# Optimization experiments

Measured on AMD Instinct MI355X. Metric: run time of the kernel, lower is better.

## Reference

```python
import jax, jax.numpy as jnp
import numpy as np

BS = 131072
NX = 4       # num_dim_x (p, theta, v, omega)
NU = 1       # num_dim_control
H = 256      # n_hidden


def segway_dynamics(x):
    # x: [bs, 4] -> f: [bs, 4], g: [bs, 4, 1]
    theta, v, omega = x[:, 1], x[:, 2], x[:, 3]
    c, s = jnp.cos(theta), jnp.sin(theta)
    f2 = (c * (9.8 * s + 11.5 * v) + 68.4 * v - 1.2 * omega ** 2 * s) / (c - 24.7)
    f3 = (-58.8 * v * c - 243.5 * v - s * (208.3 + omega ** 2 * c)) / (c ** 2 - 24.7)
    f = jnp.stack([v, omega, f2, f3], axis=1)
    g2 = (-1.8 * c - 10.9) / (c - 24.7)
    g3 = (9.3 * c + 38.6) / (c ** 2 - 24.7)
    zero = jnp.zeros_like(g2)
    g = jnp.stack([zero, zero, g2, g3], axis=1)[:, :, None]
    return f, g


def setup_inputs() -> dict:
    key = jax.random.key(0)
    ks = jax.random.split(key, 13)
    d = {"x": jax.random.normal(ks[0], (BS, NX), dtype=jnp.float32)}
    shapes = {
        "Vw1": (H, NX), "Vb1": (H,),
        "Vw2": (H, H),  "Vb2": (H,),
        "Vw3": (H // 4, H), "Vb3": (H // 4,),
        "Uw1": (H, NX), "Ub1": (H,),
        "Uw2": (H, H),  "Ub2": (H,),
        "Uw3": (NU, H), "Ub3": (NU,),
    }
    for i, (name, shp) in enumerate(shapes.items()):
        d[name] = jax.random.normal(ks[i + 1], shp, dtype=jnp.float32) * 0.05
    return d


def reference(x, Vw1, Vb1, Vw2, Vb2, Vw3, Vb3, Uw1, Ub1, Uw2, Ub2, Uw3, Ub3):
    # --- Lyapunov value + analytic gradient ---
    a1 = jnp.tanh(x @ Vw1.T + Vb1)          # [bs, H]
    a2 = jnp.tanh(a1 @ Vw2.T + Vb2)         # [bs, H]
    a3 = jnp.tanh(a2 @ Vw3.T + Vb3)         # [bs, H//4]
    V = 0.5 * jnp.sum(a3 * a3, axis=1)      # [bs]
    # diag_embed(1-tanh^2) @ W  ==  (1-tanh^2)[:, :, None] * W  (no dense diag)
    D1 = (1.0 - a1 ** 2)[:, :, None] * Vw1[None]                          # [bs, H, 4]
    D2 = (1.0 - a2 ** 2)[:, :, None] * jnp.einsum('ij,bjk->bik', Vw2, D1)  # [bs, H, 4]
    D3 = (1.0 - a3 ** 2)[:, :, None] * jnp.einsum('ij,bjk->bik', Vw3, D2)  # [bs, H/4, 4]
    grad_V = jnp.einsum('bi,bij->bj', a3, D3)  # [bs, 4]

    # --- learned controls ---
    u1 = jnp.tanh(x @ Uw1.T + Ub1)
    u2 = jnp.tanh(u1 @ Uw2.T + Ub2)
    u = jnp.tanh(u2 @ Uw3.T + Ub3) * 20.0     # [bs, 1]

    # --- Lie derivatives / Vdot ---
    f, g = segway_dynamics(x)
    L_f_V = jnp.sum(grad_V * f, axis=1, keepdims=True)    # [bs, 1]
    L_g_V = jnp.einsum('bi,bic->bc', grad_V, g)           # [bs, 1]
    Vdot = (L_f_V + jnp.sum(L_g_V * u, axis=1, keepdims=True))[:, :, None]  # [bs,1,1]
    return u, V, Vdot
```

## Files before the change

kernel.cpp:

```cpp
#include <hip/hip_runtime.h>
#include <hip/hip_bf16.h>

#define BSZ 131072

typedef __bf16 v8bf __attribute__((ext_vector_type(8)));
typedef float f32x4 __attribute__((ext_vector_type(4)));

constexpr int RPB = 32;
constexpr int MT  = RPB / 16;
constexpr int NTHREADS = 512;
constexpr int LDA = 264;

constexpr int OFF_B2T = 0;
constexpr int OFF_U2T = 65536;
constexpr int OFF_B2  = 131072;
constexpr int OFF_B3T = 196608;
constexpr int OFF_B3  = 212992;
constexpr int OFF_U3  = 229376;
constexpr int OFF_GV  = 233472;
constexpr int OFF_LV1 = 237568;
constexpr int OFF_LU1 = 245760;
constexpr int WS_ELEMS = 253952;

__device__ __forceinline__ float tanhf_fast(float x){
  float e = __builtin_amdgcn_exp2f(x * 2.885390082f);
  return __builtin_fmaf(-2.0f, __builtin_amdgcn_rcpf(e + 1.0f), 1.0f);
}

__device__ __forceinline__ __bf16 f2bf(float f){
  unsigned u = __builtin_bit_cast(unsigned, f);
  u += 0x8000u;
  unsigned short h = (unsigned short)(u >> 16);
  return __builtin_bit_cast(__bf16, h);
}

__device__ __forceinline__ unsigned pk2bf(float lo, float hi){
  unsigned r;
  asm("v_cvt_pk_bf16_f32 %0, %1, %2" : "=v"(r) : "v"(lo), "v"(hi));
  return r;
}
__device__ __forceinline__ float bflo(unsigned u){ return __builtin_bit_cast(float, u << 16); }
__device__ __forceinline__ float bfhi(unsigned u){ return __builtin_bit_cast(float, u & 0xffff0000u); }

__global__ void prep_weights(const float* __restrict__ Vw2,
                             const float* __restrict__ Uw2,
                             const float* __restrict__ Vw3,
                             const float* __restrict__ Vw1,
                             const float* __restrict__ Uw1,
                             const float* __restrict__ Uw3,
                             __bf16* __restrict__ ws){
  int e = blockIdx.x * 256 + threadIdx.x;
  if (e >= WS_ELEMS) return;
  int idx, NT, base, mode; const float* W;
  if      (e <  65536){ idx = e;          W = Vw2; mode = 0; NT = 16; base = OFF_B2T; }
  else if (e < 131072){ idx = e - 65536;  W = Uw2; mode = 0; NT = 16; base = OFF_U2T; }
  else if (e < 196608){ idx = e - 131072; W = Vw2; mode = 1; NT = 16; base = OFF_B2;  }
  else if (e < 212992){ idx = e - 196608; W = Vw3; mode = 0; NT = 4;  base = OFF_B3T; }
  else if (e < 229376){ idx = e - 212992; W = Vw3; mode = 1; NT = 16; base = OFF_B3;  }
  else if (e < 233472){ idx = e - 229376; W = Uw3; mode = 2; NT = 1;  base = OFF_U3;  }
  else if (e < 237568){ idx = e - 233472; W = Vw1; mode = 3; NT = 1;  base = OFF_GV;  }
  else if (e < 245760){ idx = e - 237568; W = Vw1; mode = 4; NT = 16; base = OFF_LV1; }
  else                { idx = e - 245760; W = Uw1; mode = 4; NT = 16; base = OFF_LU1; }
  int j = idx & 7, l = (idx >> 3) & 63, f = idx >> 9;
  int nt = f % NT, ks = f / NT;
  int k = ks * 32 + (l >> 4) * 8 + j;
  int n = nt * 16 + (l & 15);
  float v;
  if      (mode == 0) v = W[n * 256 + k];
  else if (mode == 1) v = W[k * 256 + n];
  else if (mode == 2) v = (n == 0) ? W[k] : 0.0f;
  else if (mode == 3) v = (n < 4)  ? W[k * 4 + n] : 0.0f;
  else                v = (k < 4)  ? W[n * 4 + k] : 0.0f;
  ws[base + idx] = f2bf(v);
}

__global__ __launch_bounds__(NTHREADS, 8) void fused_clf(
    const float* __restrict__ x,
    const float* __restrict__ Vb1, const float* __restrict__ Vb2,
    const float* __restrict__ Vb3,
    const float* __restrict__ Ub1, const float* __restrict__ Ub2,
    const float* __restrict__ Ub3, const float* __restrict__ Uw3,
    const __bf16* __restrict__ ws,
    float* __restrict__ out)
{
  __shared__ alignas(16) __bf16 b1[RPB][LDA];
  __shared__ alignas(16) __bf16 b2[RPB][LDA];
  __shared__ union alignas(16) S3 {
    __bf16 b3[RPB][72];
    float  r4[8][RPB][4];
  } s3;
  __shared__ alignas(16) float red[RPB][4];
  __shared__ float utile[RPB];

  const int tid  = threadIdx.x;
  const int lane = tid & 63;
  const int wave = tid >> 6;
  const int quad = lane >> 4;
  const int l16  = lane & 15;
  const int row0 = blockIdx.x * RPB;

  v8bf xa[MT];
  #pragma unroll
  for (int m = 0; m < MT; m++){
    v8bf z;
    #pragma unroll
    for (int j = 0; j < 8; j++) z[j] = (__bf16)0.0f;
    if (quad == 0){
      float4 xv = ((const float4*)x)[row0 + m*16 + l16];
      z[0] = f2bf(xv.x); z[1] = f2bf(xv.y); z[2] = f2bf(xv.z); z[3] = f2bf(xv.w);
    }
    xa[m] = z;
  }


  auto layer1m = [&](const __bf16* __restrict__ Bw, const float* __restrict__ bv,
                     __bf16 (*dst)[LDA]){
    const v8bf* B = (const v8bf*)Bw;
    v8bf bf0 = B[(wave*2 + 0)*64 + lane];
    v8bf bf1 = B[(wave*2 + 1)*64 + lane];
    f32x4 acc[MT][2];
    #pragma unroll
    for (int m = 0; m < MT; m++){ f32x4 z={0.f,0.f,0.f,0.f}; acc[m][0]=z; acc[m][1]=z; }
    __builtin_amdgcn_s_setprio(1);
    #pragma unroll
    for (int m = 0; m < MT; m++){
      acc[m][0] = __builtin_amdgcn_mfma_f32_16x16x32_bf16(bf0, xa[m], acc[m][0], 0,0,0);
      acc[m][1] = __builtin_amdgcn_mfma_f32_16x16x32_bf16(bf1, xa[m], acc[m][1], 0,0,0);
    }
    __builtin_amdgcn_s_setprio(0);
    #pragma unroll
    for (int nt = 0; nt < 2; nt++){
      const int f0 = (wave*2 + nt)*16 + quad*4;
      f32x4 bvv = ((const f32x4*)bv)[f0 >> 2];
      #pragma unroll
      for (int m = 0; m < MT; m++){
        const int brow = m*16 + l16;
        uint2 pk;
        pk.x = pk2bf(tanhf_fast(acc[m][nt][0] + bvv[0]),
                     tanhf_fast(acc[m][nt][1] + bvv[1]));
        pk.y = pk2bf(tanhf_fast(acc[m][nt][2] + bvv[2]),
                     tanhf_fast(acc[m][nt][3] + bvv[3]));
        *(uint2*)&dst[brow][f0] = pk;
      }
    }
  };

  auto gemm256 = [&](const __bf16 (*A)[LDA], const __bf16* __restrict__ Bw,
                     const float* __restrict__ bias, __bf16 (*dst)[LDA], int epi){
    f32x4 acc[MT][2];
    #pragma unroll
    for (int m = 0; m < MT; m++){ f32x4 z={0.f,0.f,0.f,0.f}; acc[m][0]=z; acc[m][1]=z; }
    const v8bf* B = (const v8bf*)Bw;
    __builtin_amdgcn_s_setprio(1);
    #pragma unroll
    for (int kk = 0; kk < 8; kk++){
      v8bf a[MT];
      #pragma unroll
      for (int m = 0; m < MT; m++)
        a[m] = *(const v8bf*)&A[m*16 + l16][kk*32 + quad*8];
      #pragma unroll
      for (int nt = 0; nt < 2; nt++){
        v8bf bf = B[(kk*16 + wave*2 + nt)*64 + lane];
        #pragma unroll
        for (int m = 0; m < MT; m++)
          acc[m][nt] = __builtin_amdgcn_mfma_f32_16x16x32_bf16(bf, a[m], acc[m][nt], 0,0,0);
      }
    }
    __builtin_amdgcn_s_setprio(0);
    #pragma unroll
    for (int nt = 0; nt < 2; nt++){
      const int f0 = (wave*2 + nt)*16 + quad*4;
      f32x4 bvv = {0.f,0.f,0.f,0.f};
      if (epi == 0) bvv = ((const f32x4*)bias)[f0 >> 2];
      #pragma unroll
      for (int m = 0; m < MT; m++){
        const int brow = m*16 + l16;
        uint2 pk;
        if (epi == 0){
          pk.x = pk2bf(tanhf_fast(acc[m][nt][0] + bvv[0]),
                       tanhf_fast(acc[m][nt][1] + bvv[1]));
          pk.y = pk2bf(tanhf_fast(acc[m][nt][2] + bvv[2]),
                       tanhf_fast(acc[m][nt][3] + bvv[3]));
        } else {
          uint2 old = *(const uint2*)&dst[brow][f0];
          float a0 = bflo(old.x), a1 = bfhi(old.x);
          float c0 = bflo(old.y), c1 = bfhi(old.y);
          pk.x = pk2bf(acc[m][nt][0] * (1.0f - a0*a0),
                       acc[m][nt][1] * (1.0f - a1*a1));
          pk.y = pk2bf(acc[m][nt][2] * (1.0f - c0*c0),
                       acc[m][nt][3] * (1.0f - c1*c1));
        }
        *(uint2*)&dst[brow][f0] = pk;
      }
    }
  };

  auto u2dot = [&](const __bf16 (*A)[LDA], const __bf16* __restrict__ Bw,
                   const float* __restrict__ bias, const float* __restrict__ w3){
    f32x4 acc[MT][2];
    #pragma unroll
    for (int m = 0; m < MT; m++){ f32x4 z={0.f,0.f,0.f,0.f}; acc[m][0]=z; acc[m][1]=z; }
    const v8bf* B = (const v8bf*)Bw;
    __builtin_amdgcn_s_setprio(1);
    #pragma unroll
    for (int kk = 0; kk < 8; kk++){
      v8bf a[MT];
      #pragma unroll
      for (int m = 0; m < MT; m++)
        a[m] = *(const v8bf*)&A[m*16 + l16][kk*32 + quad*8];
      #pragma unroll
      for (int nt = 0; nt < 2; nt++){
        v8bf bf = B[(kk*16 + wave*2 + nt)*64 + lane];
        #pragma unroll
        for (int m = 0; m < MT; m++)
          acc[m][nt] = __builtin_amdgcn_mfma_f32_16x16x32_bf16(bf, a[m], acc[m][nt], 0,0,0);
      }
    }
    __builtin_amdgcn_s_setprio(0);
    float part[MT];
    #pragma unroll
    for (int m = 0; m < MT; m++) part[m] = 0.f;
    #pragma unroll
    for (int nt = 0; nt < 2; nt++){
      const int f0 = (wave*2 + nt)*16 + quad*4;
      f32x4 bvv = ((const f32x4*)bias)[f0 >> 2];
      f32x4 w3v = ((const f32x4*)w3)[f0 >> 2];
      #pragma unroll
      for (int m = 0; m < MT; m++)
        #pragma unroll
        for (int r = 0; r < 4; r++)
          part[m] = __builtin_fmaf(tanhf_fast(acc[m][nt][r] + bvv[r]), w3v[r], part[m]);
    }
    #pragma unroll
    for (int m = 0; m < MT; m++){
      part[m] += __shfl_xor(part[m], 16);
      part[m] += __shfl_xor(part[m], 32);
    }
    if (quad == 0){
      #pragma unroll
      for (int m = 0; m < MT; m++)
        s3.r4[wave][m*16 + l16][0] = part[m];
    }
  };

  auto mfma_reduce4 = [&](const __bf16 (*A)[LDA], const __bf16* __restrict__ Bw){
    f32x4 acc[MT];
    #pragma unroll
    for (int m = 0; m < MT; m++){ f32x4 z={0.f,0.f,0.f,0.f}; acc[m]=z; }
    const v8bf* B = (const v8bf*)Bw;
    v8bf bf = B[wave*64 + lane];
    __builtin_amdgcn_s_setprio(1);
    #pragma unroll
    for (int m = 0; m < MT; m++){
      v8bf a = *(const v8bf*)&A[m*16 + l16][wave*32 + quad*8];
      acc[m] = __builtin_amdgcn_mfma_f32_16x16x32_bf16(bf, a, acc[m], 0,0,0);
    }
    __builtin_amdgcn_s_setprio(0);
    if (quad == 0){
      #pragma unroll
      for (int m = 0; m < MT; m++)
        *(f32x4*)&s3.r4[wave][m*16 + l16][0] = acc[m];
    }
  };

  layer1m(ws + OFF_LU1, Ub1, b2);
  layer1m(ws + OFF_LV1, Vb1, b1);
  __syncthreads();
  u2dot(b2, ws + OFF_U2T, Ub2, Uw3);
  __syncthreads();
  gemm256(b1, ws + OFF_B2T, Vb2, b2, 0);
  if (tid < RPB){
    float z = Ub3[0];
    #pragma unroll
    for (int w = 0; w < 8; w++) z += s3.r4[w][tid][0];
    float u = tanhf_fast(z) * 20.0f;
    utile[tid] = u;
    out[row0 + tid] = u;
  }
  __syncthreads();

  {
    const int mt = wave >> 2;
    const int nt = wave & 3;
    f32x4 acc = {0.f,0.f,0.f,0.f};
    const v8bf* B = (const v8bf*)(ws + OFF_B3T);
    __builtin_amdgcn_s_setprio(1);
    #pragma unroll
    for (int kk = 0; kk < 8; kk++){
      v8bf bf = B[(kk*4 + nt)*64 + lane];
      v8bf a = *(const v8bf*)&b2[mt*16 + l16][kk*32 + quad*8];
      acc = __builtin_amdgcn_mfma_f32_16x16x32_bf16(bf, a, acc, 0,0,0);
    }
    __builtin_amdgcn_s_setprio(0);
    const int f0 = nt*16 + quad*4;
    f32x4 bvv = ((const f32x4*)Vb3)[f0 >> 2];
    const int brow = mt*16 + l16;
    float t0 = tanhf_fast(acc[0] + bvv[0]);
    float t1 = tanhf_fast(acc[1] + bvv[1]);
    float t2 = tanhf_fast(acc[2] + bvv[2]);
    float t3 = tanhf_fast(acc[3] + bvv[3]);
    float s0 = t0*t0, s1 = t1*t1, s2 = t2*t2, s3q = t3*t3;
    float sq = (s0 + s1) + (s2 + s3q);
    sq += __shfl_xor(sq, 16);
    sq += __shfl_xor(sq, 32);
    if (quad == 0) red[brow][nt] = sq;
    uint2 pk;
    pk.x = pk2bf(t0*(1.0f - s0), t1*(1.0f - s1));
    pk.y = pk2bf(t2*(1.0f - s2), t3*(1.0f - s3q));
    *(uint2*)&s3.b3[brow][f0] = pk;
  }
  __syncthreads();

  {
    f32x4 acc[MT][2];
    #pragma unroll
    for (int m = 0; m < MT; m++){ f32x4 z={0.f,0.f,0.f,0.f}; acc[m][0]=z; acc[m][1]=z; }
    const v8bf* B = (const v8bf*)(ws + OFF_B3);
    __builtin_amdgcn_s_setprio(1);
    #pragma unroll
    for (int kk = 0; kk < 2; kk++){
      v8bf a[MT];
      #pragma unroll
      for (int m = 0; m < MT; m++)
        a[m] = *(const v8bf*)&s3.b3[m*16 + l16][kk*32 + quad*8];
      #pragma unroll
      for (int nt = 0; nt < 2; nt++){
        v8bf bf = B[(kk*16 + wave*2 + nt)*64 + lane];
        #pragma unroll
        for (int m = 0; m < MT; m++)
          acc[m][nt] = __builtin_amdgcn_mfma_f32_16x16x32_bf16(bf, a[m], acc[m][nt], 0,0,0);
      }
    }
    __builtin_amdgcn_s_setprio(0);
    #pragma unroll
    for (int nt = 0; nt < 2; nt++){
      const int f0 = (wave*2 + nt)*16 + quad*4;
      #pragma unroll
      for (int m = 0; m < MT; m++){
        const int brow = m*16 + l16;
        uint2 old = *(const uint2*)&b2[brow][f0];
        float a0 = bflo(old.x), a1 = bfhi(old.x);
        float c0 = bflo(old.y), c1 = bfhi(old.y);
        uint2 pk;
        pk.x = pk2bf(acc[m][nt][0] * (1.0f - a0*a0),
                     acc[m][nt][1] * (1.0f - a1*a1));
        pk.y = pk2bf(acc[m][nt][2] * (1.0f - c0*c0),
                     acc[m][nt][3] * (1.0f - c1*c1));
        *(uint2*)&b2[brow][f0] = pk;
      }
    }
    if (tid < RPB)
      out[BSZ + row0 + tid] = 0.5f * (red[tid][0] + red[tid][1] + red[tid][2] + red[tid][3]);
  }
  __syncthreads();

  gemm256(b2, ws + OFF_B2, nullptr, b1, 1);
  __syncthreads();
  mfma_reduce4(b1, ws + OFF_GV);
  __syncthreads();
  if (tid < RPB*4){
    int b = tid >> 2, k2 = tid & 3;
    float s = 0.f;
    #pragma unroll
    for (int w = 0; w < 8; w++) s += s3.r4[w][b][k2];
    red[b][k2] = s;
  }
  __syncthreads();

  if (tid < RPB){
    float4 xv = ((const float4*)x)[row0 + tid];
    float th = xv.y, vv = xv.z, om = xv.w;
    float c, s;
    __sincosf(th, &s, &c);
    float rdc  = __builtin_amdgcn_rcpf(c - 24.7f);
    float rdc2 = __builtin_amdgcn_rcpf(c*c - 24.7f);
    float f2v = (c*(9.8f*s + 11.5f*vv) + 68.4f*vv - 1.2f*om*om*s) * rdc;
    float f3v = (-58.8f*vv*c - 243.5f*vv - s*(208.3f + om*om*c)) * rdc2;
    float g2v = (-1.8f*c - 10.9f) * rdc;
    float g3v = (9.3f*c + 38.6f) * rdc2;
    f32x4 rv = *(const f32x4*)&red[tid][0];
    float Lf = rv[0]*vv + rv[1]*om + rv[2]*f2v + rv[3]*f3v;
    float Lg = rv[2]*g2v + rv[3]*g3v;
    out[2*BSZ + row0 + tid] = Lf + Lg * utile[tid];
  }
}

extern "C" void kernel_launch(void* const* d_in, const int* in_sizes, int n_in,
                              void* d_out, int out_size, void* d_ws, size_t ws_size,
                              hipStream_t stream) {
  const float* x   = (const float*)d_in[0];
  const float* Vw1 = (const float*)d_in[1];
  const float* Vb1 = (const float*)d_in[2];
  const float* Vw2 = (const float*)d_in[3];
  const float* Vb2 = (const float*)d_in[4];
  const float* Vw3 = (const float*)d_in[5];
  const float* Vb3 = (const float*)d_in[6];
  const float* Uw1 = (const float*)d_in[7];
  const float* Ub1 = (const float*)d_in[8];
  const float* Uw2 = (const float*)d_in[9];
  const float* Ub2 = (const float*)d_in[10];
  const float* Uw3 = (const float*)d_in[11];
  const float* Ub3 = (const float*)d_in[12];
  __bf16* ws = (__bf16*)d_ws;
  float* out = (float*)d_out;

  hipLaunchKernelGGL(prep_weights, dim3((WS_ELEMS + 255) / 256), dim3(256), 0, stream,
                     Vw2, Uw2, Vw3, Vw1, Uw1, Uw3, ws);
  hipLaunchKernelGGL(fused_clf, dim3(BSZ / RPB), dim3(NTHREADS), 0, stream,
                     x, Vb1, Vb2, Vb3, Ub1, Ub2, Ub3, Uw3, ws, out);
}
```

Measured before the change: 178.1 us.

## Double rows per block, keep a2 in registers, fuse final gradient reduction

Doubles rows per block from 32 to 64 so each wave reuses every loaded weight fragment across four M-tiles, and lowers the launch-bounds occupancy hint to 4 blocks. The bf16 a2 activations stay in registers, so the D2 epilogue no longer reads them back from shared memory. The last backward GEMM now folds the (1-a1^2)·Vw1 projection into its epilogue with fp32 Vw1, removing one barrier and the separate MFMA reduce pass. In exchange, register pressure and shared-memory use per block go up, which may lower occupancy.

After: 166.1 us. -6.7%, faster.

```diff
diff --git a/kernel.cpp b/kernel.cpp
--- a/kernel.cpp
+++ b/kernel.cpp
@@ -6,7 +6,7 @@
 typedef __bf16 v8bf __attribute__((ext_vector_type(8)));
 typedef float f32x4 __attribute__((ext_vector_type(4)));
 
-constexpr int RPB = 32;
+constexpr int RPB = 64;
 constexpr int MT  = RPB / 16;
 constexpr int NTHREADS = 512;
 constexpr int LDA = 264;
@@ -74,8 +74,8 @@
   ws[base + idx] = f2bf(v);
 }
 
-__global__ __launch_bounds__(NTHREADS, 8) void fused_clf(
-    const float* __restrict__ x,
+__global__ __launch_bounds__(NTHREADS, 4) void fused_clf(
+    const float* __restrict__ x, const float* __restrict__ Vw1f,
     const float* __restrict__ Vb1, const float* __restrict__ Vb2,
     const float* __restrict__ Vb3,
     const float* __restrict__ Ub1, const float* __restrict__ Ub2,
@@ -99,6 +99,8 @@
   const int l16  = lane & 15;
   const int row0 = blockIdx.x * RPB;
 
+  uint2 keep_a2[2*MT];
+
   v8bf xa[MT];
   #pragma unroll
   for (int m = 0; m < MT; m++){
@@ -145,8 +147,9 @@
     }
   };
 
-  auto gemm256 = [&](const __bf16 (*A)[LDA], const __bf16* __restrict__ Bw,
-                     const float* __restrict__ bias, __bf16 (*dst)[LDA], int epi){
+  auto gemm256t = [&](const __bf16 (*A)[LDA], const __bf16* __restrict__ Bw,
+                      const float* __restrict__ bias, __bf16 (*dst)[LDA],
+                      uint2* keep){
     f32x4 acc[MT][2];
     #pragma unroll
     for (int m = 0; m < MT; m++){ f32x4 z={0.f,0.f,0.f,0.f}; acc[m][0]=z; acc[m][1]=z; }
@@ -170,26 +173,16 @@
     #pragma unroll
     for (int nt = 0; nt < 2; nt++){
       const int f0 = (wave*2 + nt)*16 + quad*4;
-      f32x4 bvv = {0.f,0.f,0.f,0.f};
-      if (epi == 0) bvv = ((const f32x4*)bias)[f0 >> 2];
+      f32x4 bvv = ((const f32x4*)bias)[f0 >> 2];
       #pragma unroll
       for (int m = 0; m < MT; m++){
         const int brow = m*16 + l16;
         uint2 pk;
-        if (epi == 0){
-          pk.x = pk2bf(tanhf_fast(acc[m][nt][0] + bvv[0]),
-                       tanhf_fast(acc[m][nt][1] + bvv[1]));
-          pk.y = pk2bf(tanhf_fast(acc[m][nt][2] + bvv[2]),
-                       tanhf_fast(acc[m][nt][3] + bvv[3]));
-        } else {
-          uint2 old = *(const uint2*)&dst[brow][f0];
-          float a0 = bflo(old.x), a1 = bfhi(old.x);
-          float c0 = bflo(old.y), c1 = bfhi(old.y);
-          pk.x = pk2bf(acc[m][nt][0] * (1.0f - a0*a0),
-                       acc[m][nt][1] * (1.0f - a1*a1));
-          pk.y = pk2bf(acc[m][nt][2] * (1.0f - c0*c0),
-                       acc[m][nt][3] * (1.0f - c1*c1));
-        }
+        pk.x = pk2bf(tanhf_fast(acc[m][nt][0] + bvv[0]),
+                     tanhf_fast(acc[m][nt][1] + bvv[1]));
+        pk.y = pk2bf(tanhf_fast(acc[m][nt][2] + bvv[2]),
+                     tanhf_fast(acc[m][nt][3] + bvv[3]));
+        if (keep) keep[nt*MT + m] = pk;
         *(uint2*)&dst[brow][f0] = pk;
       }
     }
@@ -243,32 +236,12 @@
     }
   };
 
-  auto mfma_reduce4 = [&](const __bf16 (*A)[LDA], const __bf16* __restrict__ Bw){
-    f32x4 acc[MT];
-    #pragma unroll
-    for (int m = 0; m < MT; m++){ f32x4 z={0.f,0.f,0.f,0.f}; acc[m]=z; }
-    const v8bf* B = (const v8bf*)Bw;
-    v8bf bf = B[wave*64 + lane];
-    __builtin_amdgcn_s_setprio(1);
-    #pragma unroll
-    for (int m = 0; m < MT; m++){
-      v8bf a = *(const v8bf*)&A[m*16 + l16][wave*32 + quad*8];
-      acc[m] = __builtin_amdgcn_mfma_f32_16x16x32_bf16(bf, a, acc[m], 0,0,0);
-    }
-    __builtin_amdgcn_s_setprio(0);
-    if (quad == 0){
-      #pragma unroll
-      for (int m = 0; m < MT; m++)
-        *(f32x4*)&s3.r4[wave][m*16 + l16][0] = acc[m];
-    }
-  };
-
   layer1m(ws + OFF_LU1, Ub1, b2);
   layer1m(ws + OFF_LV1, Vb1, b1);
   __syncthreads();
   u2dot(b2, ws + OFF_U2T, Ub2, Uw3);
   __syncthreads();
-  gemm256(b1, ws + OFF_B2T, Vb2, b2, 0);
+  gemm256t(b1, ws + OFF_B2T, Vb2, b2, keep_a2);
   if (tid < RPB){
     float z = Ub3[0];
     #pragma unroll
@@ -280,34 +253,41 @@
   __syncthreads();
 
   {
-    const int mt = wave >> 2;
+    const int mp = wave >> 2;
     const int nt = wave & 3;
-    f32x4 acc = {0.f,0.f,0.f,0.f};
+    f32x4 acc[2];
+    { f32x4 z={0.f,0.f,0.f,0.f}; acc[0]=z; acc[1]=z; }
     const v8bf* B = (const v8bf*)(ws + OFF_B3T);
     __builtin_amdgcn_s_setprio(1);
     #pragma unroll
     for (int kk = 0; kk < 8; kk++){
       v8bf bf = B[(kk*4 + nt)*64 + lane];
-      v8bf a = *(const v8bf*)&b2[mt*16 + l16][kk*32 + quad*8];
-      acc = __builtin_amdgcn_mfma_f32_16x16x32_bf16(bf, a, acc, 0,0,0);
+      #pragma unroll
+      for (int m2 = 0; m2 < 2; m2++){
+        v8bf a = *(const v8bf*)&b2[(mp*2 + m2)*16 + l16][kk*32 + quad*8];
+        acc[m2] = __builtin_amdgcn_mfma_f32_16x16x32_bf16(bf, a, acc[m2], 0,0,0);
+      }
     }
     __builtin_amdgcn_s_setprio(0);
     const int f0 = nt*16 + quad*4;
     f32x4 bvv = ((const f32x4*)Vb3)[f0 >> 2];
-    const int brow = mt*16 + l16;
-    float t0 = tanhf_fast(acc[0] + bvv[0]);
-    float t1 = tanhf_fast(acc[1] + bvv[1]);
-    float t2 = tanhf_fast(acc[2] + bvv[2]);
-    float t3 = tanhf_fast(acc[3] + bvv[3]);
-    float s0 = t0*t0, s1 = t1*t1, s2 = t2*t2, s3q = t3*t3;
-    float sq = (s0 + s1) + (s2 + s3q);
-    sq += __shfl_xor(sq, 16);
-    sq += __shfl_xor(sq, 32);
-    if (quad == 0) red[brow][nt] = sq;
-    uint2 pk;
-    pk.x = pk2bf(t0*(1.0f - s0), t1*(1.0f - s1));
-    pk.y = pk2bf(t2*(1.0f - s2), t3*(1.0f - s3q));
-    *(uint2*)&s3.b3[brow][f0] = pk;
+    #pragma unroll
+    for (int m2 = 0; m2 < 2; m2++){
+      const int brow = (mp*2 + m2)*16 + l16;
+      float t0 = tanhf_fast(acc[m2][0] + bvv[0]);
+      float t1 = tanhf_fast(acc[m2][1] + bvv[1]);
+      float t2 = tanhf_fast(acc[m2][2] + bvv[2]);
+      float t3 = tanhf_fast(acc[m2][3] + bvv[3]);
+      float s0 = t0*t0, s1 = t1*t1, s2 = t2*t2, s3q = t3*t3;
+      float sq = (s0 + s1) + (s2 + s3q);
+      sq += __shfl_xor(sq, 16);
+      sq += __shfl_xor(sq, 32);
+      if (quad == 0) red[brow][nt] = sq;
+      uint2 pk;
+      pk.x = pk2bf(t0*(1.0f - s0), t1*(1.0f - s1));
+      pk.y = pk2bf(t2*(1.0f - s2), t3*(1.0f - s3q));
+      *(uint2*)&s3.b3[brow][f0] = pk;
+    }
   }
   __syncthreads();
 
@@ -338,7 +318,7 @@
       #pragma unroll
       for (int m = 0; m < MT; m++){
         const int brow = m*16 + l16;
-        uint2 old = *(const uint2*)&b2[brow][f0];
+        uint2 old = keep_a2[nt*MT + m];
         float a0 = bflo(old.x), a1 = bfhi(old.x);
         float c0 = bflo(old.y), c1 = bfhi(old.y);
         uint2 pk;
@@ -354,9 +334,62 @@
   }
   __syncthreads();
 
-  gemm256(b2, ws + OFF_B2, nullptr, b1, 1);
-  __syncthreads();
-  mfma_reduce4(b1, ws + OFF_GV);
+  {
+    f32x4 acc[MT][2];
+    #pragma unroll
+    for (int m = 0; m < MT; m++){ f32x4 z={0.f,0.f,0.f,0.f}; acc[m][0]=z; acc[m][1]=z; }
+    const v8bf* B = (const v8bf*)(ws + OFF_B2);
+    __builtin_amdgcn_s_setprio(1);
+    #pragma unroll
+    for (int kk = 0; kk < 8; kk++){
+      v8bf a[MT];
+      #pragma unroll
+      for (int m = 0; m < MT; m++)
+        a[m] = *(const v8bf*)&b2[m*16 + l16][kk*32 + quad*8];
+      #pragma unroll
+      for (int nt = 0; nt < 2; nt++){
+        v8bf bf = B[(kk*16 + wave*2 + nt)*64 + lane];
+        #pragma unroll
+        for (int m = 0; m < MT; m++)
+          acc[m][nt] = __builtin_amdgcn_mfma_f32_16x16x32_bf16(bf, a[m], acc[m][nt], 0,0,0);
+      }
+    }
+    __builtin_amdgcn_s_setprio(0);
+    f32x4 gp[MT];
+    #pragma unroll
+    for (int m = 0; m < MT; m++){ f32x4 z={0.f,0.f,0.f,0.f}; gp[m]=z; }
+    #pragma unroll
+    for (int nt = 0; nt < 2; nt++){
+      const int f0 = (wave*2 + nt)*16 + quad*4;
+      f32x4 vw0 = ((const f32x4*)Vw1f)[f0 + 0];
+      f32x4 vw1 = ((const f32x4*)Vw1f)[f0 + 1];
+      f32x4 vw2 = ((const f32x4*)Vw1f)[f0 + 2];
+      f32x4 vw3 = ((const f32x4*)Vw1f)[f0 + 3];
+      #pragma unroll
+      for (int m = 0; m < MT; m++){
+        uint2 old = *(const uint2*)&b1[m*16 + l16][f0];
+        float a0 = bflo(old.x), a1 = bfhi(old.x);
+        float c0 = bflo(old.y), c1 = bfhi(old.y);
+        float s0 = acc[m][nt][0] * (1.0f - a0*a0);
+        float s1 = acc[m][nt][1] * (1.0f - a1*a1);
+        float s2 = acc[m][nt][2] * (1.0f - c0*c0);
+        float s3v = acc[m][nt][3] * (1.0f - c1*c1);
+        gp[m] += s0*vw0 + s1*vw1 + s2*vw2 + s3v*vw3;
+      }
+    }
+    #pragma unroll
+    for (int m = 0; m < MT; m++){
+      #pragma unroll
+      for (int j = 0; j < 4; j++){
+        float v = gp[m][j];
+        v += __shfl_xor(v, 16);
+        v += __shfl_xor(v, 32);
+        gp[m][j] = v;
+      }
+      if (quad == 0)
+        *(f32x4*)&s3.r4[wave][m*16 + l16][0] = gp[m];
+    }
+  }
   __syncthreads();
   if (tid < RPB*4){
     int b = tid >> 2, k2 = tid & 3;
@@ -407,5 +440,5 @@
   hipLaunchKernelGGL(prep_weights, dim3((WS_ELEMS + 255) / 256), dim3(256), 0, stream,
                      Vw2, Uw2, Vw3, Vw1, Uw1, Uw3, ws);
   hipLaunchKernelGGL(fused_clf, dim3(BSZ / RPB), dim3(NTHREADS), 0, stream,
-                     x, Vb1, Vb2, Vb3, Ub1, Ub2, Ub3, Uw3, ws, out);
-}
+                     x, Vw1, Vb1, Vb2, Vb3, Ub1, Ub2, Ub3, Uw3, ws, out);
+}
```
